# Kernel tuning notes

Hardware: AMD Instinct MI355X
Metric: run time of the kernel (lower is better)

## Reference

```python
import math
import jax, jax.numpy as jnp
import numpy as np

B, S, D = 4, 4096, 1024
H = 16
DH = D // H          # 64
INNER = H * DH       # 1024
EPS = 1e-6


def _layernorm(z, g, b):
    m = jnp.mean(z, axis=-1, keepdims=True)
    v = jnp.mean((z - m) ** 2, axis=-1, keepdims=True)
    return (z - m) * jax.lax.rsqrt(v + EPS) * g + b


def _pos_encoding(seq_len, d_model, dtype):
    pos = jnp.arange(seq_len, dtype=jnp.float32)[:, None]                    # [S,1]
    div = jnp.exp(jnp.arange(0, d_model, 2, dtype=jnp.float32)
                  * (-math.log(10000.0) / d_model))                          # [D/2]
    pe = jnp.zeros((seq_len, d_model), dtype=jnp.float32)
    pe = pe.at[:, 0::2].set(jnp.sin(pos * div))
    pe = pe.at[:, 1::2].set(jnp.cos(pos * div))
    return pe.astype(dtype)[None]                                            # [1,S,D]


def setup_inputs() -> dict:
    key = jax.random.key(0)
    ks = jax.random.split(key, 8)
    std = 0.02
    x = jax.random.normal(ks[0], (B, S, D), dtype=jnp.float32)
    inp = {
        "x": x,
        "ln1_g": jnp.ones((D,), jnp.float32),
        "ln1_b": jnp.zeros((D,), jnp.float32),
        "Wqkv": std * jax.random.normal(ks[1], (D, 3 * INNER), jnp.float32),
        "Wo": std * jax.random.normal(ks[2], (INNER, D), jnp.float32),
        "bo": jnp.zeros((D,), jnp.float32),
        "ln2_g": jnp.ones((D,), jnp.float32),
        "ln2_b": jnp.zeros((D,), jnp.float32),
        "W1": std * jax.random.normal(ks[3], (D, D), jnp.float32),
        "b1": jnp.zeros((D,), jnp.float32),
        "W2": std * jax.random.normal(ks[4], (D, D), jnp.float32),
        "b2": jnp.zeros((D,), jnp.float32),
    }
    return inp


def reference(x, ln1_g, ln1_b, Wqkv, Wo, bo, ln2_g, ln2_b, W1, b1, W2, b2):
    # --- ln_1 + positional encoding (dropout p=0) ---
    h = _layernorm(x, ln1_g, ln1_b)
    h = h + _pos_encoding(h.shape[1], h.shape[2], h.dtype)
    # --- linear self-attention (non-causal, efficient attention) ---
    qkv = h @ Wqkv                                                           # [B,S,3*INNER]
    q, k, v = jnp.split(qkv, 3, axis=-1)
    def heads(t):  # [B,S,INNER] -> [B,H,S,DH]
        return t.reshape(B, S, H, DH).transpose(0, 2, 1, 3)
    q, k, v = heads(q), heads(k), heads(v)
    q = jax.nn.softmax(q, axis=-1) * (DH ** -0.5)
    k = jax.nn.softmax(k, axis=-2)
    ctx = jnp.einsum("bhnd,bhne->bhde", k, v)                               # [B,H,DH,DH]
    attn_out = jnp.einsum("bhnd,bhde->bhne", q, ctx)                        # [B,H,S,DH]
    attn_out = attn_out.transpose(0, 2, 1, 3).reshape(B, S, INNER)
    attn_out = attn_out @ Wo + bo
    # --- residual, ln_2, MLP (Linear -> GELU -> Linear), residual ---
    x = x + attn_out
    y = _layernorm(x, ln2_g, ln2_b)
    y = jax.nn.gelu(y @ W1 + b1, approximate=False) @ W2 + b2
    return x + y
```

## Files before the change

### kernel.cpp

```cpp
#include <hip/hip_runtime.h>
#include <hip/hip_bf16.h>
#include <math.h>

#define B_   4
#define S_   4096
#define D_   1024
#define H_   16
#define DH_  64
#define BS_  (B_ * S_)
#define N3_  3072

using bf16 = __hip_bfloat16;
typedef __attribute__((ext_vector_type(8))) short bf16x8;
typedef __attribute__((ext_vector_type(4))) float f32x4;

#define GAS __attribute__((address_space(1)))
#define LAS __attribute__((address_space(3)))

__device__ __forceinline__ void gload_lds16(const bf16* g, bf16* l) {
  __builtin_amdgcn_global_load_lds((const GAS void*)g, (LAS void*)l, 16, 0, 0);
}

__device__ __forceinline__ float bf2f(short u) {
  unsigned int x = ((unsigned int)(unsigned short)u) << 16;
  return __builtin_bit_cast(float, x);
}
__device__ __forceinline__ unsigned short f2bfu(float f) {
  bf16 t = __float2bfloat16(f);
  return *(unsigned short*)&t;
}

__global__ __launch_bounds__(256)
void prep_kernel(const float* __restrict__ x, const float* __restrict__ ln1_g,
                 const float* __restrict__ ln1_b, bf16* __restrict__ h,
                 const float* __restrict__ Wqkv, const float* __restrict__ Wo,
                 const float* __restrict__ W1, const float* __restrict__ W2,
                 bf16* __restrict__ wqkvt, bf16* __restrict__ wot,
                 bf16* __restrict__ w1t, bf16* __restrict__ w2t)
{
  int bid = blockIdx.x;
  int t = threadIdx.x;
  if (bid < BS_) {
    int row = bid;
    float4 v = ((const float4*)(x + (size_t)row * D_))[t];
    float s  = v.x + v.y + v.z + v.w;
    float ss = v.x * v.x + v.y * v.y + v.z * v.z + v.w * v.w;
#pragma unroll
    for (int o = 32; o > 0; o >>= 1) { s += __shfl_xor(s, o); ss += __shfl_xor(ss, o); }
    __shared__ float red[8];
    int wid = t >> 6, lane = t & 63;
    if (lane == 0) { red[wid] = s; red[4 + wid] = ss; }
    __syncthreads();
    s  = red[0] + red[1] + red[2] + red[3];
    ss = red[4] + red[5] + red[6] + red[7];
    float mean = s * (1.0f / D_);
    float var  = ss * (1.0f / D_) - mean * mean;
    float rs   = rsqrtf(var + 1e-6f);
    int d0 = t * 4;
    const float4 g4 = ((const float4*)ln1_g)[t];
    const float4 b4 = ((const float4*)ln1_b)[t];
    float o0 = (v.x - mean) * rs * g4.x + b4.x;
    float o1 = (v.y - mean) * rs * g4.y + b4.y;
    float o2 = (v.z - mean) * rs * g4.z + b4.z;
    float o3 = (v.w - mean) * rs * g4.w + b4.w;
    const float C = -0.0089944730194f;
    float p = (float)(row & (S_ - 1));
    float sn, cs;
    __sincosf(p * __expf((float)d0 * C), &sn, &cs);        o0 += sn; o1 += cs;
    __sincosf(p * __expf((float)(d0 + 2) * C), &sn, &cs);  o2 += sn; o3 += cs;
    ushort4 pk;
    pk.x = f2bfu(o0); pk.y = f2bfu(o1); pk.z = f2bfu(o2); pk.w = f2bfu(o3);
    ((ushort4*)h)[(size_t)row * (D_ / 4) + t] = pk;
  } else {
    int e = bid - BS_;
    int gx = e % 192, ky = e / 192;
    __shared__ float tile[32][33];
    const float* W; bf16* Wt; int N, xo;
    if (gx < 96)        { W = Wqkv; Wt = wqkvt; N = N3_; xo = gx; }
    else if (gx < 128)  { W = Wo;   Wt = wot;   N = D_;  xo = gx - 96; }
    else if (gx < 160)  { W = W1;   Wt = w1t;   N = D_;  xo = gx - 128; }
    else                { W = W2;   Wt = w2t;   N = D_;  xo = gx - 160; }
    int n0 = xo * 32, k0 = ky * 32;
    int tx = t & 31, ty = t >> 5;
#pragma unroll
    for (int j = 0; j < 32; j += 8)
      tile[ty + j][tx] = W[(size_t)(k0 + ty + j) * N + n0 + tx];
    __syncthreads();
#pragma unroll
    for (int j = 0; j < 32; j += 8)
      Wt[(size_t)(n0 + ty + j) * 1024 + k0 + tx] = __float2bfloat16(tile[tx][ty + j]);
  }
}

__global__ __launch_bounds__(256)
void ln_kernel(const bf16* __restrict__ Xb, const float* __restrict__ G,
               const float* __restrict__ Bv, bf16* __restrict__ out)
{
  int row = blockIdx.x;
  int t = threadIdx.x;
  ushort4 u = ((const ushort4*)Xb)[(size_t)row * (D_ / 4) + t];
  float4 v;
  v.x = bf2f(u.x); v.y = bf2f(u.y); v.z = bf2f(u.z); v.w = bf2f(u.w);
  float s  = v.x + v.y + v.z + v.w;
  float ss = v.x * v.x + v.y * v.y + v.z * v.z + v.w * v.w;
#pragma unroll
  for (int o = 32; o > 0; o >>= 1) { s += __shfl_xor(s, o); ss += __shfl_xor(ss, o); }
  __shared__ float red[8];
  int wid = t >> 6, lane = t & 63;
  if (lane == 0) { red[wid] = s; red[4 + wid] = ss; }
  __syncthreads();
  s  = red[0] + red[1] + red[2] + red[3];
  ss = red[4] + red[5] + red[6] + red[7];
  float mean = s * (1.0f / D_);
  float var  = ss * (1.0f / D_) - mean * mean;
  float rs   = rsqrtf(var + 1e-6f);
  const float4 g4 = ((const float4*)G)[t];
  const float4 b4 = ((const float4*)Bv)[t];
  ushort4 pk;
  pk.x = f2bfu((v.x - mean) * rs * g4.x + b4.x);
  pk.y = f2bfu((v.y - mean) * rs * g4.y + b4.y);
  pk.z = f2bfu((v.z - mean) * rs * g4.z + b4.z);
  pk.w = f2bfu((v.w - mean) * rs * g4.w + b4.w);
  ((ushort4*)out)[(size_t)row * (D_ / 4) + t] = pk;
}

enum { EPI_QKV = 0, EPI_BIAS_RES_BF16 = 1, EPI_BIAS_GELU_BF16 = 2, EPI_BIAS_RESB_F32 = 3 };

#define MFMA_ __builtin_amdgcn_mfma_f32_16x16x32_bf16

template<int EPI, bool AHM>
__global__ __launch_bounds__(512)
void gemm256(const bf16* __restrict__ A, const bf16* __restrict__ Bt,
             float* __restrict__ Cf, bf16* __restrict__ Cb,
             const float* __restrict__ bias, const float* __restrict__ resf,
             const bf16* __restrict__ resb,
             bf16* __restrict__ Ck, bf16* __restrict__ Cv,
             int M, int N, int K)
{
  extern __shared__ __align__(16) char smem[];
  bf16* lds = (bf16*)smem;

  const int t = threadIdx.x;
  const int wid = t >> 6, lane = t & 63;
  const int wr = wid >> 2, wc = wid & 3;
  const int bid = blockIdx.x;
  const int c = bid & 7;
  const int w = bid >> 3;
  const int sst = w >> 4;
  const int ii = w & 15;
  const int txg = sst >> 1, tyg = sst & 1;
  const int iy = ii & 3, ix = ii >> 2;
  const int ty = c * 8 + tyg * 4 + iy;
  const int tx = txg * 4 + ix;
  const int m0 = ty << 8, n0 = tx << 8;

  const bf16* Ab = AHM
      ? A + (((size_t)(m0 >> 12) * 16) * 4096 + (m0 & 4095)) * 64
      : A + (size_t)m0 * K;
  const bf16* Bb = Bt + (size_t)n0 * K;

  const int srow = t >> 2;
  const int scol = (((t & 3) ^ ((t >> 3) & 3)) * 8);
  const int NT = K >> 6;
  const int fr = lane & 15;
  const int fksw = (((lane >> 4) ^ ((lane >> 1) & 3)) * 8);

  f32x4 acc[8][4] = {};

  #define LDSHALF(b, mat, kh) (lds + (((((b) << 1) + (mat)) << 1) + (kh)) * 8192)

  #define STAGE(bkt, akt, mat, kh) do {                                        \
    bf16* _dst = LDSHALF((bkt) & 1, (mat), (kh)) + t * 8;                      \
    const int _ktk = (akt);                                                    \
    if ((mat) == 0 && AHM) {                                                   \
      const bf16* _sb = Ab + (size_t)_ktk * 262144 + (size_t)srow * 64         \
                        + (kh) * 32 + scol;                                    \
      gload_lds16(_sb, _dst);                                                  \
      gload_lds16(_sb + 8192, _dst + 4096);                                    \
    } else {                                                                   \
      const bf16* _sb = ((mat) == 0 ? Ab : Bb) + (size_t)srow * K              \
                        + (_ktk << 6) + (kh) * 32 + scol;                      \
      gload_lds16(_sb, _dst);                                                  \
      gload_lds16(_sb + (size_t)128 * K, _dst + 4096);                         \
    }                                                                          \
  } while (0)

  STAGE(0, 0, 0, 0); STAGE(0, 0, 1, 0);
  STAGE(0, 0, 0, 1); STAGE(0, 0, 1, 1);
  asm volatile("s_waitcnt vmcnt(4)" ::: "memory");
  __builtin_amdgcn_s_barrier();

#pragma unroll 2
  for (int kt = 0; kt < NT; ++kt) {
    const int cur = kt & 1;
    const int nk = (kt + 1 < NT) ? (kt + 1) : (NT - 1);
    const bf16* hA0 = LDSHALF(cur, 0, 0);
    const bf16* hB0 = LDSHALF(cur, 1, 0);
    const bf16* hA1 = LDSHALF(cur, 0, 1);
    const bf16* hB1 = LDSHALF(cur, 1, 1);
    bf16x8 a[8], b0, b1, b2, b3;

#pragma unroll
    for (int mi = 0; mi < 8; ++mi)
      a[mi] = *(const bf16x8*)&hA0[(wr * 128 + mi * 16 + fr) * 32 + fksw];
    b0 = *(const bf16x8*)&hB0[(wc * 64 +  0 + fr) * 32 + fksw];
    b1 = *(const bf16x8*)&hB0[(wc * 64 + 16 + fr) * 32 + fksw];
    STAGE(kt + 1, nk, 0, 0);
    __builtin_amdgcn_s_barrier();
    __builtin_amdgcn_s_setprio(1);
#pragma unroll
    for (int mi = 0; mi < 8; ++mi) {
      acc[mi][0] = MFMA_(a[mi], b0, acc[mi][0], 0, 0, 0);
      acc[mi][1] = MFMA_(a[mi], b1, acc[mi][1], 0, 0, 0);
    }
    __builtin_amdgcn_s_setprio(0);
    __builtin_amdgcn_s_barrier();

    b2 = *(const bf16x8*)&hB0[(wc * 64 + 32 + fr) * 32 + fksw];
    b3 = *(const bf16x8*)&hB0[(wc * 64 + 48 + fr) * 32 + fksw];
    STAGE(kt + 1, nk, 1, 0);
    __builtin_amdgcn_s_barrier();
    __builtin_amdgcn_s_setprio(1);
#pragma unroll
    for (int mi = 0; mi < 8; ++mi) {
      acc[mi][2] = MFMA_(a[mi], b2, acc[mi][2], 0, 0, 0);
      acc[mi][3] = MFMA_(a[mi], b3, acc[mi][3], 0, 0, 0);
    }
    __builtin_amdgcn_s_setprio(0);
    asm volatile("s_waitcnt vmcnt(4)" ::: "memory");
    __builtin_amdgcn_s_barrier();

#pragma unroll
    for (int mi = 0; mi < 8; ++mi)
      a[mi] = *(const bf16x8*)&hA1[(wr * 128 + mi * 16 + fr) * 32 + fksw];
    b0 = *(const bf16x8*)&hB1[(wc * 64 +  0 + fr) * 32 + fksw];
    b1 = *(const bf16x8*)&hB1[(wc * 64 + 16 + fr) * 32 + fksw];
    STAGE(kt + 1, nk, 0, 1);
    __builtin_amdgcn_s_barrier();
    __builtin_amdgcn_s_setprio(1);
#pragma unroll
    for (int mi = 0; mi < 8; ++mi) {
      acc[mi][0] = MFMA_(a[mi], b0, acc[mi][0], 0, 0, 0);
      acc[mi][1] = MFMA_(a[mi], b1, acc[mi][1], 0, 0, 0);
    }
    __builtin_amdgcn_s_setprio(0);
    __builtin_amdgcn_s_barrier();

    b2 = *(const bf16x8*)&hB1[(wc * 64 + 32 + fr) * 32 + fksw];
    b3 = *(const bf16x8*)&hB1[(wc * 64 + 48 + fr) * 32 + fksw];
    STAGE(kt + 1, nk, 1, 1);
    __builtin_amdgcn_s_barrier();
    __builtin_amdgcn_s_setprio(1);
#pragma unroll
    for (int mi = 0; mi < 8; ++mi) {
      acc[mi][2] = MFMA_(a[mi], b2, acc[mi][2], 0, 0, 0);
      acc[mi][3] = MFMA_(a[mi], b3, acc[mi][3], 0, 0, 0);
    }
    __builtin_amdgcn_s_setprio(0);
    asm volatile("s_waitcnt vmcnt(4)" ::: "memory");
    __builtin_amdgcn_s_barrier();
  }
  asm volatile("s_waitcnt vmcnt(0)" ::: "memory");

  unsigned short* ot = (unsigned short*)lds;

  const bool q_repack = (EPI == EPI_QKV) && (n0 < 1024);
  if (EPI != EPI_QKV || q_repack) {
#pragma unroll
    for (int mi = 0; mi < 8; ++mi) {
#pragma unroll
      for (int ni = 0; ni < 4; ++ni) {
#pragma unroll
        for (int j = 0; j < 4; ++j) {
          int row = wr * 128 + mi * 16 + (lane >> 4) * 4 + j;
          int col = wc * 64 + ni * 16 + fr;
          int u = col >> 3;
          int st = (u & ~7) | ((u ^ row) & 7);
          ot[row * 256 + st * 8 + (col & 7)] = f2bfu(acc[mi][ni][j]);
        }
      }
    }
    __syncthreads();
  }

  if (EPI == EPI_QKV) {
    const int brow = m0 >> 12;
    const int mrow = m0 & 4095;
    if (q_repack) {
      int tq = t & 3, trow = t >> 2;
#pragma unroll
      for (int p = 0; p < 2; ++p) {
        int row = p * 128 + trow;
        int sglob = mrow + row;
#pragma unroll
        for (int i = 0; i < 8; ++i) {
          int uu = i * 4 + tq;
          int hl = uu >> 3, k = uu & 7;
          int st = (uu & ~7) | ((uu ^ row) & 7);
          bf16x8 v = *(const bf16x8*)&ot[row * 256 + st * 8];
          unsigned short* dst = (unsigned short*)Cb +
            (((size_t)(brow * 16 + (n0 >> 6) + hl) * 4096 + sglob) * 64 + k * 8);
          *(bf16x8*)dst = v;
        }
      }
    } else {
      int qsel = n0 >> 10;
#pragma unroll
      for (int mi = 0; mi < 8; ++mi) {
        int sloc = mrow + wr * 128 + mi * 16 + (lane >> 4) * 4;
#pragma unroll
        for (int ni = 0; ni < 4; ++ni) {
          int col = n0 + wc * 64 + ni * 16 + fr;
          int hh = (col >> 6) & 15;
          int dd = col & 63;
          unsigned short* kp = (unsigned short*)(qsel == 1 ? Ck : Cv) +
            (((size_t)(brow * 16 + hh) * 64 + dd) * 4096 + sloc);
          ushort4 pk;
          pk.x = f2bfu(acc[mi][ni][0]); pk.y = f2bfu(acc[mi][ni][1]);
          pk.z = f2bfu(acc[mi][ni][2]); pk.w = f2bfu(acc[mi][ni][3]);
          *(ushort4*)kp = pk;
        }
      }
    }
  } else {
    int rlane = lane & 31;
    int rrow0 = lane >> 5;
    float bias8[8];
    *(float4*)&bias8[0] = *(const float4*)&bias[n0 + rlane * 8];
    *(float4*)&bias8[4] = *(const float4*)&bias[n0 + rlane * 8 + 4];
#pragma unroll 4
    for (int it = 0; it < 16; ++it) {
      int row = wid * 32 + it * 2 + rrow0;
      int st = (rlane & ~7) | ((rlane ^ row) & 7);
      bf16x8 v8 = *(const bf16x8*)&ot[row * 256 + st * 8];
      int grow = m0 + row;
      float o[8];
#pragma unroll
      for (int q = 0; q < 8; ++q) o[q] = bf2f(v8[q]) + bias8[q];
      if (EPI == EPI_BIAS_RES_BF16) {
        const float* rp = resf + (size_t)grow * N + n0 + rlane * 8;
        float4 r0 = *(const float4*)rp, r1 = *(const float4*)(rp + 4);
        o[0] += r0.x; o[1] += r0.y; o[2] += r0.z; o[3] += r0.w;
        o[4] += r1.x; o[5] += r1.y; o[6] += r1.z; o[7] += r1.w;
        bf16x8 wv;
#pragma unroll
        for (int q = 0; q < 8; ++q) wv[q] = (short)f2bfu(o[q]);
        *(bf16x8*)((unsigned short*)Cb + (size_t)grow * N + n0 + rlane * 8) = wv;
      } else if (EPI == EPI_BIAS_GELU_BF16) {
        bf16x8 wv;
#pragma unroll
        for (int q = 0; q < 8; ++q) {
          float u = o[q];
          u = 0.5f * u * (1.0f + erff(u * 0.70710678118654752f));
          wv[q] = (short)f2bfu(u);
        }
        *(bf16x8*)((unsigned short*)Cb + (size_t)grow * N + n0 + rlane * 8) = wv;
      } else {
        const unsigned short* rp = (const unsigned short*)resb + (size_t)grow * N + n0 + rlane * 8;
        bf16x8 r8 = *(const bf16x8*)rp;
#pragma unroll
        for (int q = 0; q < 8; ++q) o[q] += bf2f(r8[q]);
        float4 s0, s1;
        s0.x = o[0]; s0.y = o[1]; s0.z = o[2]; s0.w = o[3];
        s1.x = o[4]; s1.y = o[5]; s1.z = o[6]; s1.w = o[7];
        float* op = Cf + (size_t)grow * N + n0 + rlane * 8;
        *(float4*)op = s0;
        *(float4*)(op + 4) = s1;
      }
    }
  }
  #undef STAGE
  #undef LDSHALF
}

__global__ __launch_bounds__(256)
void ctx_partial(const bf16* __restrict__ kT, const bf16* __restrict__ vT,
                 float* __restrict__ pctx, float* __restrict__ pden)
{
  int blk = blockIdx.x;
  int kc = blk & 7, bh = blk >> 3;
  int t = threadIdx.x, lane = t & 63, wid = t >> 6;
  const int fr = lane & 15, g = lane >> 4;
  __shared__ float part[4][4096];
  __shared__ float dpart[4][64];

  f32x4 acc[4][4] = {};
  float dsum[4] = {0.f, 0.f, 0.f, 0.f};
  const unsigned short* kb = (const unsigned short*)kT + (size_t)bh * 64 * 4096;
  const unsigned short* vb = (const unsigned short*)vT + (size_t)bh * 64 * 4096;
  const int kbase = kc * 512 + wid * 128;
#pragma unroll
  for (int i = 0; i < 4; ++i) {
    int kofs = kbase + i * 32 + g * 8;
    bf16x8 av[4], bv[4];
#pragma unroll
    for (int mi = 0; mi < 4; ++mi) {
      bf16x8 kr = *(const bf16x8*)(kb + (size_t)(mi * 16 + fr) * 4096 + kofs);
      bf16x8 ae;
      float es = 0.f;
#pragma unroll
      for (int j = 0; j < 8; ++j) {
        float e = __expf(bf2f(kr[j]));
        es += e;
        ae[j] = (short)f2bfu(e);
      }
      dsum[mi] += es;
      av[mi] = ae;
      bv[mi] = *(const bf16x8*)(vb + (size_t)(mi * 16 + fr) * 4096 + kofs);
    }
#pragma unroll
    for (int mi = 0; mi < 4; ++mi)
#pragma unroll
      for (int ni = 0; ni < 4; ++ni)
        acc[mi][ni] = MFMA_(av[mi], bv[ni], acc[mi][ni], 0, 0, 0);
  }
#pragma unroll
  for (int mi = 0; mi < 4; ++mi) {
    dsum[mi] += __shfl_xor(dsum[mi], 16);
    dsum[mi] += __shfl_xor(dsum[mi], 32);
  }
#pragma unroll
  for (int mi = 0; mi < 4; ++mi)
#pragma unroll
    for (int ni = 0; ni < 4; ++ni)
      *(f32x4*)&part[wid][(mi * 4 + ni) * 256 + lane * 4] = acc[mi][ni];
  if (g == 0) {
#pragma unroll
    for (int mi = 0; mi < 4; ++mi) dpart[wid][mi * 16 + fr] = dsum[mi];
  }
  __syncthreads();
  int lane2 = t & 63, fg = t >> 6;
#pragma unroll
  for (int ff = 0; ff < 4; ++ff) {
    int f = fg * 4 + ff;
    f32x4 s = {};
#pragma unroll
    for (int ww = 0; ww < 4; ++ww)
      s += *(const f32x4*)&part[ww][f * 256 + lane2 * 4];
    *(f32x4*)&pctx[((size_t)blk * 16 + f) * 256 + lane2 * 4] = s;
  }
  if (t < 64)
    pden[blk * 64 + t] = dpart[0][t] + dpart[1][t] + dpart[2][t] + dpart[3][t];
}

__global__ __launch_bounds__(256)
void ctx_merge(const float* __restrict__ pctx, const float* __restrict__ pden,
               bf16* __restrict__ ctxT)
{
  int bh = blockIdx.x;
  int t = threadIdx.x, lane2 = t & 63, fg = t >> 6;
  __shared__ float rden[64];
  if (t < 64) {
    float s = 0.f;
    for (int kc = 0; kc < 8; ++kc) s += pden[(bh * 8 + kc) * 64 + t];
    rden[t] = 1.0f / s;
  }
  __syncthreads();
  int fr2 = lane2 & 15, g2 = lane2 >> 4;
#pragma unroll
  for (int ff = 0; ff < 4; ++ff) {
    int f = fg * 4 + ff;
    int mi = f >> 2, ni = f & 3;
    f32x4 s = {};
#pragma unroll
    for (int kc = 0; kc < 8; ++kc)
      s += *(const f32x4*)&pctx[(((size_t)(bh * 8 + kc)) * 16 + f) * 256 + lane2 * 4];
    int e = ni * 16 + fr2;
    int d0 = mi * 16 + g2 * 4;
    ushort4 pk;
    pk.x = f2bfu(s[0] * rden[d0 + 0]);
    pk.y = f2bfu(s[1] * rden[d0 + 1]);
    pk.z = f2bfu(s[2] * rden[d0 + 2]);
    pk.w = f2bfu(s[3] * rden[d0 + 3]);
    *(ushort4*)((unsigned short*)ctxT + ((size_t)bh * 64 + e) * 64 + d0) = pk;
  }
}

__global__ __launch_bounds__(256)
void attn_kernel(const bf16* __restrict__ qhm, const bf16* __restrict__ ctxT,
                 bf16* __restrict__ attn)
{
  int blk = blockIdx.x;
  int chunk = blk & 15, bh = blk >> 4;
  int t = threadIdx.x, lane = t & 63, wid = t >> 6;
  __shared__ bf16 P[256 * 64];
  __shared__ bf16 CT[64 * 64];

  {
    const unsigned short* cg = (const unsigned short*)ctxT + (size_t)bh * 4096;
#pragma unroll
    for (int r = 0; r < 2; ++r) {
      int idx = r * 256 + t;
      int e = idx >> 3, b = idx & 7;
      bf16x8 v = *(const bf16x8*)(cg + idx * 8);
      *(bf16x8*)&CT[e * 64 + ((b ^ (e & 7)) * 8)] = v;
    }
  }
  {
    int s = chunk * 256 + t;
    const unsigned short* qp = (const unsigned short*)qhm + ((size_t)bh * 4096 + s) * 64;
    float p[64];
#pragma unroll
    for (int j = 0; j < 8; ++j) {
      bf16x8 q8 = *(const bf16x8*)(qp + j * 8);
#pragma unroll
      for (int i = 0; i < 8; ++i) p[j * 8 + i] = bf2f(q8[i]);
    }
    float mx = p[0];
#pragma unroll
    for (int d = 1; d < 64; ++d) mx = fmaxf(mx, p[d]);
    float sum = 0.f;
#pragma unroll
    for (int d = 0; d < 64; ++d) { p[d] = __expf(p[d] - mx); sum += p[d]; }
    float f = 0.125f / sum;
    bf16* pb = &P[(t >> 6) * 4096 + (t & 63) * 64];
#pragma unroll
    for (int b = 0; b < 8; ++b) {
      bf16x8 pk;
#pragma unroll
      for (int i = 0; i < 8; ++i) pk[i] = (short)f2bfu(p[b * 8 + i] * f);
      *(bf16x8*)&pb[((b ^ (t & 7)) * 8)] = pk;
    }
  }
  __syncthreads();

  const int fr = lane & 15, g = lane >> 4;
  f32x4 acc[4][4] = {};
  const bf16* Pw = &P[wid * 4096];
#pragma unroll
  for (int ks = 0; ks < 2; ++ks) {
    bf16x8 av[4], bv[4];
#pragma unroll
    for (int mi = 0; mi < 4; ++mi) {
      int r = mi * 16 + fr;
      av[mi] = *(const bf16x8*)&Pw[r * 64 + (((ks * 4 + g) ^ (r & 7)) * 8)];
    }
#pragma unroll
    for (int ni = 0; ni < 4; ++ni) {
      int e = ni * 16 + fr;
      bv[ni] = *(const bf16x8*)&CT[e * 64 + (((ks * 4 + g) ^ (e & 7)) * 8)];
    }
#pragma unroll
    for (int mi = 0; mi < 4; ++mi)
#pragma unroll
      for (int ni = 0; ni < 4; ++ni)
        acc[mi][ni] = MFMA_(av[mi], bv[ni], acc[mi][ni], 0, 0, 0);
  }
  unsigned short* ob = (unsigned short*)attn +
      ((size_t)bh * 4096 + chunk * 256 + wid * 64) * 64;
#pragma unroll
  for (int mi = 0; mi < 4; ++mi)
#pragma unroll
    for (int ni = 0; ni < 4; ++ni) {
      int e = ni * 16 + fr;
#pragma unroll
      for (int j = 0; j < 4; ++j) {
        int r = mi * 16 + g * 4 + j;
        ob[(size_t)r * 64 + e] = f2bfu(acc[mi][ni][j]);
      }
    }
}

#define OFF_WQKVT  ((size_t)0)
#define OFF_WOT    ((size_t)6291456)
#define OFF_W1T    ((size_t)8388608)
#define OFF_W2T    ((size_t)10485760)
#define OFF_CTXT   ((size_t)12582912)
#define OFF_PCTX   ((size_t)13631488)
#define OFF_PDEN   ((size_t)22020096)
#define OFF_ATTN   ((size_t)33554432)
#define OFF_H      OFF_ATTN
#define OFF_QHM    ((size_t)67108864)
#define OFF_KT     ((size_t)100663296)
#define OFF_VT     ((size_t)134217728)
#define OFF_Z      OFF_QHM
#define OFF_X2B    OFF_KT
#define OFF_Y      OFF_VT

extern "C" void kernel_launch(void* const* d_in, const int* in_sizes, int n_in,
                              void* d_out, int out_size, void* d_ws, size_t ws_size,
                              hipStream_t stream)
{
  const float* x     = (const float*)d_in[0];
  const float* ln1_g = (const float*)d_in[1];
  const float* ln1_b = (const float*)d_in[2];
  const float* Wqkv  = (const float*)d_in[3];
  const float* Wo    = (const float*)d_in[4];
  const float* bo    = (const float*)d_in[5];
  const float* ln2_g = (const float*)d_in[6];
  const float* ln2_b = (const float*)d_in[7];
  const float* W1    = (const float*)d_in[8];
  const float* b1    = (const float*)d_in[9];
  const float* W2    = (const float*)d_in[10];
  const float* b2    = (const float*)d_in[11];
  float* out = (float*)d_out;
  char* ws = (char*)d_ws;

  bf16*  h     = (bf16*)(ws + OFF_H);
  bf16*  attn  = (bf16*)(ws + OFF_ATTN);
  bf16*  qhm   = (bf16*)(ws + OFF_QHM);
  bf16*  kT    = (bf16*)(ws + OFF_KT);
  bf16*  vT    = (bf16*)(ws + OFF_VT);
  bf16*  ctxT  = (bf16*)(ws + OFF_CTXT);
  float* pctx  = (float*)(ws + OFF_PCTX);
  float* pden  = (float*)(ws + OFF_PDEN);
  bf16*  x2b   = (bf16*)(ws + OFF_X2B);
  bf16*  y     = (bf16*)(ws + OFF_Y);
  bf16*  z     = (bf16*)(ws + OFF_Z);
  bf16*  wqkvt = (bf16*)(ws + OFF_WQKVT);
  bf16*  wot   = (bf16*)(ws + OFF_WOT);
  bf16*  w1t   = (bf16*)(ws + OFF_W1T);
  bf16*  w2t   = (bf16*)(ws + OFF_W2T);

  const size_t GEMM_LDS = 131072;

  prep_kernel<<<BS_ + 192 * 32, 256, 0, stream>>>(
      x, ln1_g, ln1_b, h, Wqkv, Wo, W1, W2, wqkvt, wot, w1t, w2t);

  gemm256<EPI_QKV, false><<<(N3_ / 256) * (BS_ / 256), 512, GEMM_LDS, stream>>>(
      h, wqkvt, nullptr, qhm, nullptr, nullptr, nullptr, kT, vT, BS_, N3_, D_);

  ctx_partial<<<512, 256, 0, stream>>>(kT, vT, pctx, pden);
  ctx_merge<<<64, 256, 0, stream>>>(pctx, pden, ctxT);

  attn_kernel<<<1024, 256, 0, stream>>>(qhm, ctxT, attn);

  gemm256<EPI_BIAS_RES_BF16, true><<<(D_ / 256) * (BS_ / 256), 512, GEMM_LDS, stream>>>(
      attn, wot, nullptr, x2b, bo, x, nullptr, nullptr, nullptr, BS_, D_, D_);

  ln_kernel<<<BS_, 256, 0, stream>>>(x2b, ln2_g, ln2_b, y);

  gemm256<EPI_BIAS_GELU_BF16, false><<<(D_ / 256) * (BS_ / 256), 512, GEMM_LDS, stream>>>(
      y, w1t, nullptr, z, b1, nullptr, nullptr, nullptr, nullptr, BS_, D_, D_);

  gemm256<EPI_BIAS_RESB_F32, false><<<(D_ / 256) * (BS_ / 256), 512, GEMM_LDS, stream>>>(
      z, w2t, out, nullptr, b2, nullptr, x2b, nullptr, nullptr, BS_, D_, D_);
}
```

Before: 350.7 us.

## Add dedicated 4-wave QKV GEMM with 128x128 per-wave tiles

Replaces the 8-wave templated GEMM for the QKV projection with a separate 256-thread kernel. Each wave computes a 128x128 output tile with an 8x8 MFMA accumulator array and simpler double-buffered staging that waits for all loads each iteration. The larger per-wave tile raises register reuse of A/B fragments and cuts LDS reads per MFMA, at the cost of much higher register pressure (256 accumulator VGPRs), one block per CU and a less finely interleaved load/compute schedule. The generic GEMM drops its QKV epilogue path.

New measurement: 377.2 us. 1.08x slower.

```diff
diff --git a/kernel.cpp b/kernel.cpp
--- a/kernel.cpp
+++ b/kernel.cpp
@@ -128,14 +128,138 @@
 
 #define MFMA_ __builtin_amdgcn_mfma_f32_16x16x32_bf16
 
+__global__ __launch_bounds__(256, 1)
+void gemm256q4(const bf16* __restrict__ A, const bf16* __restrict__ Bt,
+               bf16* __restrict__ Cq, bf16* __restrict__ Ck, bf16* __restrict__ Cv,
+               int M, int N, int K)
+{
+  extern __shared__ __align__(16) char smem[];
+  bf16* lds = (bf16*)smem;
+
+  const int t = threadIdx.x;
+  const int wid = t >> 6, lane = t & 63;
+  const int wr = wid >> 1, wc = wid & 1;
+  const int bid = blockIdx.x;
+  const int c = bid & 7;
+  const int w = bid >> 3;
+  const int sst = w >> 4;
+  const int ii = w & 15;
+  const int txg = sst >> 1, tyg = sst & 1;
+  const int iy = ii & 3, ix = ii >> 2;
+  const int ty = c * 8 + tyg * 4 + iy;
+  const int tx = txg * 4 + ix;
+  const int m0 = ty << 8, n0 = tx << 8;
+
+  const bf16* Ab = A + (size_t)m0 * K;
+  const bf16* Bb = Bt + (size_t)n0 * K;
+
+  const int NT = K >> 6;
+  const int fr = lane & 15;
+  const int fksw = (((lane >> 4) ^ ((lane >> 1) & 3)) * 8);
+  const int srow = t >> 2;
+  const int scol = (((t & 3) ^ ((t >> 3) & 3)) * 8);
+
+  f32x4 acc[8][8] = {};
+
+  #define LDSHALF(b, mat, kh) (lds + (((((b) << 1) + (mat)) << 1) + (kh)) * 8192)
+  #define STAGEQ(bkt, akt, mat, kh) do {                                       \
+    bf16* _dst = LDSHALF((bkt) & 1, (mat), (kh)) + t * 8;                      \
+    const bf16* _sb = ((mat) == 0 ? Ab : Bb) + (size_t)srow * K                \
+                      + ((akt) << 6) + (kh) * 32 + scol;                       \
+    gload_lds16(_sb,                    _dst);                                 \
+    gload_lds16(_sb + (size_t)64 * K,   _dst + 2048);                          \
+    gload_lds16(_sb + (size_t)128 * K,  _dst + 4096);                          \
+    gload_lds16(_sb + (size_t)192 * K,  _dst + 6144);                          \
+  } while (0)
+
+  STAGEQ(0, 0, 0, 0); STAGEQ(0, 0, 1, 0); STAGEQ(0, 0, 0, 1); STAGEQ(0, 0, 1, 1);
+  asm volatile("s_waitcnt vmcnt(0)" ::: "memory");
+  __builtin_amdgcn_s_barrier();
+
+  for (int kt = 0; kt < NT; ++kt) {
+    const int cur = kt & 1;
+    const int nk = (kt + 1 < NT) ? (kt + 1) : (NT - 1);
+    STAGEQ(kt + 1, nk, 0, 0); STAGEQ(kt + 1, nk, 1, 0);
+    STAGEQ(kt + 1, nk, 0, 1); STAGEQ(kt + 1, nk, 1, 1);
+#pragma unroll
+    for (int kh = 0; kh < 2; ++kh) {
+      const bf16* hA = LDSHALF(cur, 0, kh);
+      const bf16* hB = LDSHALF(cur, 1, kh);
+      bf16x8 a[8], b[8];
+#pragma unroll
+      for (int mi = 0; mi < 8; ++mi)
+        a[mi] = *(const bf16x8*)&hA[(wr * 128 + mi * 16 + fr) * 32 + fksw];
+#pragma unroll
+      for (int ni = 0; ni < 8; ++ni)
+        b[ni] = *(const bf16x8*)&hB[(wc * 128 + ni * 16 + fr) * 32 + fksw];
+      __builtin_amdgcn_s_setprio(1);
+#pragma unroll
+      for (int mi = 0; mi < 8; ++mi)
+#pragma unroll
+        for (int ni = 0; ni < 8; ++ni)
+          acc[mi][ni] = MFMA_(a[mi], b[ni], acc[mi][ni], 0, 0, 0);
+      __builtin_amdgcn_s_setprio(0);
+    }
+    asm volatile("s_waitcnt vmcnt(0)" ::: "memory");
+    __builtin_amdgcn_s_barrier();
+  }
+
+  const int brow = m0 >> 12;
+  const int mrow = m0 & 4095;
+  if (n0 < 1024) {
+    unsigned short* ot = (unsigned short*)lds;
+#pragma unroll
+    for (int mi = 0; mi < 8; ++mi) {
+#pragma unroll
+      for (int ni = 0; ni < 8; ++ni) {
+#pragma unroll
+        for (int j = 0; j < 4; ++j) {
+          int row = wr * 128 + mi * 16 + (lane >> 4) * 4 + j;
+          int col = wc * 128 + ni * 16 + fr;
+          int u = col >> 3;
+          int st = (u & ~7) | ((u ^ row) & 7);
+          ot[row * 256 + st * 8 + (col & 7)] = f2bfu(acc[mi][ni][j]);
+        }
+      }
+    }
+    __syncthreads();
+    int sglob = mrow + t;
+#pragma unroll 8
+    for (int uu = 0; uu < 32; ++uu) {
+      int st = (uu & ~7) | ((uu ^ t) & 7);
+      bf16x8 v = *(const bf16x8*)&ot[t * 256 + st * 8];
+      int hl = uu >> 3, k8 = uu & 7;
+      *(bf16x8*)((unsigned short*)Cq +
+        (((size_t)(brow * 16 + (n0 >> 6) + hl) * 4096 + sglob) * 64 + k8 * 8)) = v;
+    }
+  } else {
+    int qsel = n0 >> 10;
+    unsigned short* base = (unsigned short*)(qsel == 1 ? Ck : Cv);
+#pragma unroll
+    for (int mi = 0; mi < 8; ++mi) {
+      int sloc = mrow + wr * 128 + mi * 16 + (lane >> 4) * 4;
+#pragma unroll
+      for (int ni = 0; ni < 8; ++ni) {
+        int col = n0 + wc * 128 + ni * 16 + fr;
+        int hh = (col >> 6) & 15;
+        int dd = col & 63;
+        ushort4 pk;
+        pk.x = f2bfu(acc[mi][ni][0]); pk.y = f2bfu(acc[mi][ni][1]);
+        pk.z = f2bfu(acc[mi][ni][2]); pk.w = f2bfu(acc[mi][ni][3]);
+        *(ushort4*)(base + (((size_t)(brow * 16 + hh) * 64 + dd) * 4096 + sloc)) = pk;
+      }
+    }
+  }
+  #undef STAGEQ
+  #undef LDSHALF
+}
+
 template<int EPI, bool AHM>
 __global__ __launch_bounds__(512)
 void gemm256(const bf16* __restrict__ A, const bf16* __restrict__ Bt,
              float* __restrict__ Cf, bf16* __restrict__ Cb,
              const float* __restrict__ bias, const float* __restrict__ resf,
-             const bf16* __restrict__ resb,
-             bf16* __restrict__ Ck, bf16* __restrict__ Cv,
-             int M, int N, int K)
+             const bf16* __restrict__ resb, int M, int N, int K)
 {
   extern __shared__ __align__(16) char smem[];
   bf16* lds = (bf16*)smem;
@@ -168,7 +292,6 @@
   f32x4 acc[8][4] = {};
 
   #define LDSHALF(b, mat, kh) (lds + (((((b) << 1) + (mat)) << 1) + (kh)) * 8192)
-
   #define STAGE(bkt, akt, mat, kh) do {                                        \
     bf16* _dst = LDSHALF((bkt) & 1, (mat), (kh)) + t * 8;                      \
     const int _ktk = (akt);                                                    \
@@ -263,110 +386,65 @@
   asm volatile("s_waitcnt vmcnt(0)" ::: "memory");
 
   unsigned short* ot = (unsigned short*)lds;
-
-  const bool q_repack = (EPI == EPI_QKV) && (n0 < 1024);
-  if (EPI != EPI_QKV || q_repack) {
-#pragma unroll
-    for (int mi = 0; mi < 8; ++mi) {
-#pragma unroll
-      for (int ni = 0; ni < 4; ++ni) {
-#pragma unroll
-        for (int j = 0; j < 4; ++j) {
-          int row = wr * 128 + mi * 16 + (lane >> 4) * 4 + j;
-          int col = wc * 64 + ni * 16 + fr;
-          int u = col >> 3;
-          int st = (u & ~7) | ((u ^ row) & 7);
-          ot[row * 256 + st * 8 + (col & 7)] = f2bfu(acc[mi][ni][j]);
-        }
+#pragma unroll
+  for (int mi = 0; mi < 8; ++mi) {
+#pragma unroll
+    for (int ni = 0; ni < 4; ++ni) {
+#pragma unroll
+      for (int j = 0; j < 4; ++j) {
+        int row = wr * 128 + mi * 16 + (lane >> 4) * 4 + j;
+        int col = wc * 64 + ni * 16 + fr;
+        int u = col >> 3;
+        int st = (u & ~7) | ((u ^ row) & 7);
+        ot[row * 256 + st * 8 + (col & 7)] = f2bfu(acc[mi][ni][j]);
       }
     }
-    __syncthreads();
-  }
-
-  if (EPI == EPI_QKV) {
-    const int brow = m0 >> 12;
-    const int mrow = m0 & 4095;
-    if (q_repack) {
-      int tq = t & 3, trow = t >> 2;
-#pragma unroll
-      for (int p = 0; p < 2; ++p) {
-        int row = p * 128 + trow;
-        int sglob = mrow + row;
-#pragma unroll
-        for (int i = 0; i < 8; ++i) {
-          int uu = i * 4 + tq;
-          int hl = uu >> 3, k = uu & 7;
-          int st = (uu & ~7) | ((uu ^ row) & 7);
-          bf16x8 v = *(const bf16x8*)&ot[row * 256 + st * 8];
-          unsigned short* dst = (unsigned short*)Cb +
-            (((size_t)(brow * 16 + (n0 >> 6) + hl) * 4096 + sglob) * 64 + k * 8);
-          *(bf16x8*)dst = v;
-        }
+  }
+  __syncthreads();
+
+  int rlane = lane & 31;
+  int rrow0 = lane >> 5;
+  float bias8[8];
+  *(float4*)&bias8[0] = *(const float4*)&bias[n0 + rlane * 8];
+  *(float4*)&bias8[4] = *(const float4*)&bias[n0 + rlane * 8 + 4];
+#pragma unroll 4
+  for (int it = 0; it < 16; ++it) {
+    int row = wid * 32 + it * 2 + rrow0;
+    int st = (rlane & ~7) | ((rlane ^ row) & 7);
+    bf16x8 v8 = *(const bf16x8*)&ot[row * 256 + st * 8];
+    int grow = m0 + row;
+    float o[8];
+#pragma unroll
+    for (int q = 0; q < 8; ++q) o[q] = bf2f(v8[q]) + bias8[q];
+    if (EPI == EPI_BIAS_RES_BF16) {
+      const float* rp = resf + (size_t)grow * N + n0 + rlane * 8;
+      float4 r0 = *(const float4*)rp, r1 = *(const float4*)(rp + 4);
+      o[0] += r0.x; o[1] += r0.y; o[2] += r0.z; o[3] += r0.w;
+      o[4] += r1.x; o[5] += r1.y; o[6] += r1.z; o[7] += r1.w;
+      bf16x8 wv;
+#pragma unroll
+      for (int q = 0; q < 8; ++q) wv[q] = (short)f2bfu(o[q]);
+      *(bf16x8*)((unsigned short*)Cb + (size_t)grow * N + n0 + rlane * 8) = wv;
+    } else if (EPI == EPI_BIAS_GELU_BF16) {
+      bf16x8 wv;
+#pragma unroll
+      for (int q = 0; q < 8; ++q) {
+        float u = o[q];
+        u = 0.5f * u * (1.0f + erff(u * 0.70710678118654752f));
+        wv[q] = (short)f2bfu(u);
       }
+      *(bf16x8*)((unsigned short*)Cb + (size_t)grow * N + n0 + rlane * 8) = wv;
     } else {
-      int qsel = n0 >> 10;
-#pragma unroll
-      for (int mi = 0; mi < 8; ++mi) {
-        int sloc = mrow + wr * 128 + mi * 16 + (lane >> 4) * 4;
-#pragma unroll
-        for (int ni = 0; ni < 4; ++ni) {
-          int col = n0 + wc * 64 + ni * 16 + fr;
-          int hh = (col >> 6) & 15;
-          int dd = col & 63;
-          unsigned short* kp = (unsigned short*)(qsel == 1 ? Ck : Cv) +
-            (((size_t)(brow * 16 + hh) * 64 + dd) * 4096 + sloc);
-          ushort4 pk;
-          pk.x = f2bfu(acc[mi][ni][0]); pk.y = f2bfu(acc[mi][ni][1]);
-          pk.z = f2bfu(acc[mi][ni][2]); pk.w = f2bfu(acc[mi][ni][3]);
-          *(ushort4*)kp = pk;
-        }
-      }
-    }
-  } else {
-    int rlane = lane & 31;
-    int rrow0 = lane >> 5;
-    float bias8[8];
-    *(float4*)&bias8[0] = *(const float4*)&bias[n0 + rlane * 8];
-    *(float4*)&bias8[4] = *(const float4*)&bias[n0 + rlane * 8 + 4];
-#pragma unroll 4
-    for (int it = 0; it < 16; ++it) {
-      int row = wid * 32 + it * 2 + rrow0;
-      int st = (rlane & ~7) | ((rlane ^ row) & 7);
-      bf16x8 v8 = *(const bf16x8*)&ot[row * 256 + st * 8];
-      int grow = m0 + row;
-      float o[8];
-#pragma unroll
-      for (int q = 0; q < 8; ++q) o[q] = bf2f(v8[q]) + bias8[q];
-      if (EPI == EPI_BIAS_RES_BF16) {
-        const float* rp = resf + (size_t)grow * N + n0 + rlane * 8;
-        float4 r0 = *(const float4*)rp, r1 = *(const float4*)(rp + 4);
-        o[0] += r0.x; o[1] += r0.y; o[2] += r0.z; o[3] += r0.w;
-        o[4] += r1.x; o[5] += r1.y; o[6] += r1.z; o[7] += r1.w;
-        bf16x8 wv;
-#pragma unroll
-        for (int q = 0; q < 8; ++q) wv[q] = (short)f2bfu(o[q]);
-        *(bf16x8*)((unsigned short*)Cb + (size_t)grow * N + n0 + rlane * 8) = wv;
-      } else if (EPI == EPI_BIAS_GELU_BF16) {
-        bf16x8 wv;
-#pragma unroll
-        for (int q = 0; q < 8; ++q) {
-          float u = o[q];
-          u = 0.5f * u * (1.0f + erff(u * 0.70710678118654752f));
-          wv[q] = (short)f2bfu(u);
-        }
-        *(bf16x8*)((unsigned short*)Cb + (size_t)grow * N + n0 + rlane * 8) = wv;
-      } else {
-        const unsigned short* rp = (const unsigned short*)resb + (size_t)grow * N + n0 + rlane * 8;
-        bf16x8 r8 = *(const bf16x8*)rp;
-#pragma unroll
-        for (int q = 0; q < 8; ++q) o[q] += bf2f(r8[q]);
-        float4 s0, s1;
-        s0.x = o[0]; s0.y = o[1]; s0.z = o[2]; s0.w = o[3];
-        s1.x = o[4]; s1.y = o[5]; s1.z = o[6]; s1.w = o[7];
-        float* op = Cf + (size_t)grow * N + n0 + rlane * 8;
-        *(float4*)op = s0;
-        *(float4*)(op + 4) = s1;
-      }
+      const unsigned short* rp = (const unsigned short*)resb + (size_t)grow * N + n0 + rlane * 8;
+      bf16x8 r8 = *(const bf16x8*)rp;
+#pragma unroll
+      for (int q = 0; q < 8; ++q) o[q] += bf2f(r8[q]);
+      float4 s0, s1;
+      s0.x = o[0]; s0.y = o[1]; s0.z = o[2]; s0.w = o[3];
+      s1.x = o[4]; s1.y = o[5]; s1.z = o[6]; s1.w = o[7];
+      float* op = Cf + (size_t)grow * N + n0 + rlane * 8;
+      *(float4*)op = s0;
+      *(float4*)(op + 4) = s1;
     }
   }
   #undef STAGE
@@ -617,8 +695,8 @@
   prep_kernel<<<BS_ + 192 * 32, 256, 0, stream>>>(
       x, ln1_g, ln1_b, h, Wqkv, Wo, W1, W2, wqkvt, wot, w1t, w2t);
 
-  gemm256<EPI_QKV, false><<<(N3_ / 256) * (BS_ / 256), 512, GEMM_LDS, stream>>>(
-      h, wqkvt, nullptr, qhm, nullptr, nullptr, nullptr, kT, vT, BS_, N3_, D_);
+  gemm256q4<<<(N3_ / 256) * (BS_ / 256), 256, GEMM_LDS, stream>>>(
+      h, wqkvt, qhm, kT, vT, BS_, N3_, D_);
 
   ctx_partial<<<512, 256, 0, stream>>>(kT, vT, pctx, pden);
   ctx_merge<<<64, 256, 0, stream>>>(pctx, pden, ctxT);
@@ -626,13 +704,13 @@
   attn_kernel<<<1024, 256, 0, stream>>>(qhm, ctxT, attn);
 
   gemm256<EPI_BIAS_RES_BF16, true><<<(D_ / 256) * (BS_ / 256), 512, GEMM_LDS, stream>>>(
-      attn, wot, nullptr, x2b, bo, x, nullptr, nullptr, nullptr, BS_, D_, D_);
+      attn, wot, nullptr, x2b, bo, x, nullptr, BS_, D_, D_);
 
   ln_kernel<<<BS_, 256, 0, stream>>>(x2b, ln2_g, ln2_b, y);
 
   gemm256<EPI_BIAS_GELU_BF16, false><<<(D_ / 256) * (BS_ / 256), 512, GEMM_LDS, stream>>>(
-      y, w1t, nullptr, z, b1, nullptr, nullptr, nullptr, nullptr, BS_, D_, D_);
+      y, w1t, nullptr, z, b1, nullptr, nullptr, BS_, D_, D_);
 
   gemm256<EPI_BIAS_RESB_F32, false><<<(D_ / 256) * (BS_ / 256), 512, GEMM_LDS, stream>>>(
-      z, w2t, out, nullptr, b2, nullptr, x2b, nullptr, nullptr, BS_, D_, D_);
-}
+      z, w2t, out, nullptr, b2, nullptr, x2b, BS_, D_, D_);
+}
```
